# Kernel optimization log

Measured on AMD Instinct MI355X. Metric: run time of the kernel, lower is better.

## Reference

```python
import jax, jax.numpy as jnp
import numpy as np

ENT_SIZE = 1_000_000
REL_SIZE = 1_000
ENT_DIM = 128
REL_DIM = 128  # == ENT_DIM, so eye(rel_dim, ent_dim) is the identity
BATCH = 262_144
MARGIN = 1.0
EPS = 1e-6  # nn.PairwiseDistance default eps, added to the difference


def setup_inputs() -> dict:
    key = jax.random.key(0)
    k1, k2, k3, k4, k5, k6, k7, k8 = jax.random.split(key, 8)
    scale = 0.05
    ent_emb = jax.random.normal(k1, (ENT_SIZE, ENT_DIM), jnp.float32) * scale
    ent_map_emb = jax.random.normal(k2, (ENT_SIZE, ENT_DIM), jnp.float32) * scale
    rel_emb = jax.random.normal(k3, (REL_SIZE, REL_DIM), jnp.float32) * scale
    rel_map_emb = jax.random.normal(k4, (REL_SIZE, REL_DIM), jnp.float32) * scale

    def make_triples(ke, kr):
        ents = jax.random.randint(ke, (BATCH, 2), 0, ENT_SIZE, jnp.int32)
        rels = jax.random.randint(kr, (BATCH, 1), 0, REL_SIZE, jnp.int32)
        # columns: head, relation, tail
        return jnp.concatenate([ents[:, :1], rels, ents[:, 1:]], axis=1)

    pos_x = make_triples(k5, k6)
    neg_x = make_triples(k7, k8)
    return {
        "ent_emb": ent_emb,
        "ent_map_emb": ent_map_emb,
        "rel_emb": rel_emb,
        "rel_map_emb": rel_map_emb,
        "pos_x": pos_x,
        "neg_x": neg_x,
    }


def _score(ent_emb, ent_map_emb, rel_emb, rel_map_emb, triple):
    h, r, t = triple[:, 0], triple[:, 1], triple[:, 2]
    head = ent_emb[h]          # [B, D]
    headp = ent_map_emb[h]     # [B, D]
    tail = ent_emb[t]
    tailp = ent_map_emb[t]
    rel = rel_emb[r]           # [B, D]
    relp = rel_map_emb[r]      # [B, D]
    # Mrh = relp[:, :, None] @ headp[:, None, :] + I ; Mrh @ head
    # == relp * <headp, head> + head   (since REL_DIM == ENT_DIM => I@head = head)
    head_proj = relp * jnp.sum(headp * head, axis=-1, keepdims=True) + head
    tail_proj = relp * jnp.sum(tailp * tail, axis=-1, keepdims=True) + tail
    d = head_proj + rel - tail_proj + EPS  # PairwiseDistance adds eps to diff
    return jnp.sqrt(jnp.sum(d * d, axis=-1))  # L2 norm (l_regular=2), [B]


def reference(ent_emb, ent_map_emb, rel_emb, rel_map_emb, pos_x, neg_x):
    pos_score = _score(ent_emb, ent_map_emb, rel_emb, rel_map_emb, pos_x)
    neg_score = _score(ent_emb, ent_map_emb, rel_emb, rel_map_emb, neg_x)
    size = pos_x.shape[0]
    return jnp.sum(jax.nn.relu(pos_score - neg_score + MARGIN)) / size
```

## Files before the change

kernel.cpp:

```cpp
#include <hip/hip_runtime.h>

#define ENT_DIM 128
#define BATCH 262144
#define MARGIN 1.0f
#define EPS 1e-6f

__global__ void zero_out_kernel(float* out) {
    out[0] = 0.0f;
}

__global__ __launch_bounds__(256) void transd_kernel(
    const float* __restrict__ ent_emb,
    const float* __restrict__ ent_map,
    const float* __restrict__ rel_emb,
    const float* __restrict__ rel_map,
    const int* __restrict__ pos_x,
    const int* __restrict__ neg_x,
    float* __restrict__ out)
{
    const int lane = threadIdx.x & 63;
    const int wid  = threadIdx.x >> 6;
    const int gwave  = blockIdx.x * 4 + wid;
    const int nwaves = gridDim.x * 4;

    float acc = 0.0f;

    for (int i = gwave; i < BATCH; i += nwaves) {
        const int ib = __builtin_amdgcn_readfirstlane(i);

        const int ph = pos_x[3 * ib + 0];
        const int pr = pos_x[3 * ib + 1];
        const int pt = pos_x[3 * ib + 2];
        const int nh = neg_x[3 * ib + 0];
        const int nr = neg_x[3 * ib + 1];
        const int nt = neg_x[3 * ib + 2];

        const float2 phe = ((const float2*)(ent_emb + (size_t)ph * ENT_DIM))[lane];
        const float2 phm = ((const float2*)(ent_map + (size_t)ph * ENT_DIM))[lane];
        const float2 pte = ((const float2*)(ent_emb + (size_t)pt * ENT_DIM))[lane];
        const float2 ptm = ((const float2*)(ent_map + (size_t)pt * ENT_DIM))[lane];
        const float2 pre = ((const float2*)(rel_emb + (size_t)pr * ENT_DIM))[lane];
        const float2 prm = ((const float2*)(rel_map + (size_t)pr * ENT_DIM))[lane];

        const float2 nhe = ((const float2*)(ent_emb + (size_t)nh * ENT_DIM))[lane];
        const float2 nhm = ((const float2*)(ent_map + (size_t)nh * ENT_DIM))[lane];
        const float2 nte = ((const float2*)(ent_emb + (size_t)nt * ENT_DIM))[lane];
        const float2 ntm = ((const float2*)(ent_map + (size_t)nt * ENT_DIM))[lane];
        const float2 nre = ((const float2*)(rel_emb + (size_t)nr * ENT_DIM))[lane];
        const float2 nrm = ((const float2*)(rel_map + (size_t)nr * ENT_DIM))[lane];

        float dph = phm.x * phe.x + phm.y * phe.y;
        float dpt = ptm.x * pte.x + ptm.y * pte.y;
        float dnh = nhm.x * nhe.x + nhm.y * nhe.y;
        float dnt = ntm.x * nte.x + ntm.y * nte.y;

        #pragma unroll
        for (int off = 32; off >= 1; off >>= 1) {
            dph += __shfl_xor(dph, off);
            dpt += __shfl_xor(dpt, off);
            dnh += __shfl_xor(dnh, off);
            dnt += __shfl_xor(dnt, off);
        }

        float dpx = prm.x * dph + phe.x + pre.x - (prm.x * dpt + pte.x) + EPS;
        float dpy = prm.y * dph + phe.y + pre.y - (prm.y * dpt + pte.y) + EPS;
        float dnx = nrm.x * dnh + nhe.x + nre.x - (nrm.x * dnt + nte.x) + EPS;
        float dny = nrm.y * dnh + nhe.y + nre.y - (nrm.y * dnt + nte.y) + EPS;

        float sp = dpx * dpx + dpy * dpy;
        float sn = dnx * dnx + dny * dny;

        #pragma unroll
        for (int off = 32; off >= 1; off >>= 1) {
            sp += __shfl_xor(sp, off);
            sn += __shfl_xor(sn, off);
        }

        float v = sqrtf(sp) - sqrtf(sn) + MARGIN;
        acc += fmaxf(v, 0.0f);
    }

    __shared__ float wsum[4];
    if (lane == 0) wsum[wid] = acc;
    __syncthreads();
    if (threadIdx.x == 0) {
        float s = wsum[0] + wsum[1] + wsum[2] + wsum[3];
        atomicAdd(out, s * (1.0f / (float)BATCH));
    }
}

extern "C" void kernel_launch(void* const* d_in, const int* in_sizes, int n_in,
                              void* d_out, int out_size, void* d_ws, size_t ws_size,
                              hipStream_t stream) {
    const float* ent_emb     = (const float*)d_in[0];
    const float* ent_map_emb = (const float*)d_in[1];
    const float* rel_emb     = (const float*)d_in[2];
    const float* rel_map_emb = (const float*)d_in[3];
    const int*   pos_x       = (const int*)d_in[4];
    const int*   neg_x       = (const int*)d_in[5];
    float* out = (float*)d_out;

    hipLaunchKernelGGL(zero_out_kernel, dim3(1), dim3(1), 0, stream, out);

    hipLaunchKernelGGL(transd_kernel, dim3(4096), dim3(256), 0, stream,
                       ent_emb, ent_map_emb, rel_emb, rel_map_emb,
                       pos_x, neg_x, out);
}
```

Baseline: 936.2 us.

## Split wave into pos/neg halves with float4 loads and double-buffered prefetch

Each wave now handles one triple per half-wave: lanes 0-31 take the positive triple and lanes 32-63 the negative one, and each lane loads float4 slices. The wave loads all 16 triples' indices for its contiguous chunk in one vector load and hands them out by shuffle. Embedding loads for the next iteration are issued before the current pair is computed, which keeps more gathers in flight to hide latency. In exchange register pressure rises from the doubled buffers, and the grid is now fixed by batch size instead of a grid-stride loop.

```diff
diff --git a/kernel.cpp b/kernel.cpp
--- a/kernel.cpp
+++ b/kernel.cpp
@@ -4,12 +4,58 @@
 #define BATCH 262144
 #define MARGIN 1.0f
 #define EPS 1e-6f
+#define NITER 16
+#define WAVES_PER_BLOCK 4
+#define NWAVES (BATCH / NITER)
+#define NBLOCKS (NWAVES / WAVES_PER_BLOCK)
 
 __global__ void zero_out_kernel(float* out) {
     out[0] = 0.0f;
 }
 
-__global__ __launch_bounds__(256) void transd_kernel(
+__device__ __forceinline__ float pair_term(
+    float4 H, float4 Hp, float4 T, float4 Tp, float4 R, float4 Rp, int lane)
+{
+    float dh = H.x*Hp.x + H.y*Hp.y + H.z*Hp.z + H.w*Hp.w;
+    float dt = T.x*Tp.x + T.y*Tp.y + T.z*Tp.z + T.w*Tp.w;
+#pragma unroll
+    for (int off = 16; off >= 1; off >>= 1) {
+        dh += __shfl_xor(dh, off);
+        dt += __shfl_xor(dt, off);
+    }
+
+    float dx = Rp.x * dh + H.x + R.x - (Rp.x * dt + T.x) + EPS;
+    float dy = Rp.y * dh + H.y + R.y - (Rp.y * dt + T.y) + EPS;
+    float dz = Rp.z * dh + H.z + R.z - (Rp.z * dt + T.z) + EPS;
+    float dw = Rp.w * dh + H.w + R.w - (Rp.w * dt + T.w) + EPS;
+
+    float s = dx*dx + dy*dy + dz*dz + dw*dw;
+#pragma unroll
+    for (int off = 16; off >= 1; off >>= 1) s += __shfl_xor(s, off);
+
+    float so = __shfl_xor(s, 32);
+    float a = sqrtf(s), b = sqrtf(so);
+    float v = (lane < 32) ? (a - b) : (b - a);
+    return fmaxf(v + MARGIN, 0.0f);
+}
+
+#define LOADP(kk, p) do {                                                   \
+    const int e0 = 3*(kk), e1 = 3*(kk) + 1, e2 = 3*(kk) + 2;                \
+    int ih = __shfl((e0 & 1) ? ivy : ivx, (e0 >> 1) + hi32);                \
+    int ir = __shfl((e1 & 1) ? ivy : ivx, (e1 >> 1) + hi32);                \
+    int it = __shfl((e2 & 1) ? ivy : ivx, (e2 >> 1) + hi32);                \
+    uint ho = ((uint)ih << 9) | lofs;                                       \
+    uint ro = ((uint)ir << 9) | lofs;                                       \
+    uint to = ((uint)it << 9) | lofs;                                       \
+    H##p  = *(const float4*)(eb + ho);                                      \
+    Hp##p = *(const float4*)(em + ho);                                      \
+    T##p  = *(const float4*)(eb + to);                                      \
+    Tp##p = *(const float4*)(em + to);                                      \
+    R##p  = *(const float4*)(rb + ro);                                      \
+    Rp##p = *(const float4*)(rm + ro);                                      \
+} while (0)
+
+__global__ __launch_bounds__(256, 4) void transd_kernel(
     const float* __restrict__ ent_emb,
     const float* __restrict__ ent_map,
     const float* __restrict__ rel_emb,
@@ -20,67 +66,39 @@
 {
     const int lane = threadIdx.x & 63;
     const int wid  = threadIdx.x >> 6;
-    const int gwave  = blockIdx.x * 4 + wid;
-    const int nwaves = gridDim.x * 4;
+    const int gw   = blockIdx.x * WAVES_PER_BLOCK + wid;
 
+    const int  hi32 = lane & 32;
+    const uint lofs = (uint)(lane & 31) << 4;
+
+    const char* __restrict__ eb = (const char*)ent_emb;
+    const char* __restrict__ em = (const char*)ent_map;
+    const char* __restrict__ rb = (const char*)rel_emb;
+    const char* __restrict__ rm = (const char*)rel_map;
+
+    int ivx = 0, ivy = 0;
+    if (lane < 24) {
+        int2 t = ((const int2*)(pos_x + 3 * NITER * gw))[lane];
+        ivx = t.x; ivy = t.y;
+    } else if (hi32 && lane < 56) {
+        int2 t = ((const int2*)(neg_x + 3 * NITER * gw))[lane - 32];
+        ivx = t.x; ivy = t.y;
+    }
+
+    float4 H0, Hp0, T0, Tp0, R0, Rp0;
+    float4 H1, Hp1, T1, Tp1, R1, Rp1;
     float acc = 0.0f;
 
-    for (int i = gwave; i < BATCH; i += nwaves) {
-        const int ib = __builtin_amdgcn_readfirstlane(i);
-
-        const int ph = pos_x[3 * ib + 0];
-        const int pr = pos_x[3 * ib + 1];
-        const int pt = pos_x[3 * ib + 2];
-        const int nh = neg_x[3 * ib + 0];
-        const int nr = neg_x[3 * ib + 1];
-        const int nt = neg_x[3 * ib + 2];
-
-        const float2 phe = ((const float2*)(ent_emb + (size_t)ph * ENT_DIM))[lane];
-        const float2 phm = ((const float2*)(ent_map + (size_t)ph * ENT_DIM))[lane];
-        const float2 pte = ((const float2*)(ent_emb + (size_t)pt * ENT_DIM))[lane];
-        const float2 ptm = ((const float2*)(ent_map + (size_t)pt * ENT_DIM))[lane];
-        const float2 pre = ((const float2*)(rel_emb + (size_t)pr * ENT_DIM))[lane];
-        const float2 prm = ((const float2*)(rel_map + (size_t)pr * ENT_DIM))[lane];
-
-        const float2 nhe = ((const float2*)(ent_emb + (size_t)nh * ENT_DIM))[lane];
-        const float2 nhm = ((const float2*)(ent_map + (size_t)nh * ENT_DIM))[lane];
-        const float2 nte = ((const float2*)(ent_emb + (size_t)nt * ENT_DIM))[lane];
-        const float2 ntm = ((const float2*)(ent_map + (size_t)nt * ENT_DIM))[lane];
-        const float2 nre = ((const float2*)(rel_emb + (size_t)nr * ENT_DIM))[lane];
-        const float2 nrm = ((const float2*)(rel_map + (size_t)nr * ENT_DIM))[lane];
-
-        float dph = phm.x * phe.x + phm.y * phe.y;
-        float dpt = ptm.x * pte.x + ptm.y * pte.y;
-        float dnh = nhm.x * nhe.x + nhm.y * nhe.y;
-        float dnt = ntm.x * nte.x + ntm.y * nte.y;
-
-        #pragma unroll
-        for (int off = 32; off >= 1; off >>= 1) {
-            dph += __shfl_xor(dph, off);
-            dpt += __shfl_xor(dpt, off);
-            dnh += __shfl_xor(dnh, off);
-            dnt += __shfl_xor(dnt, off);
-        }
-
-        float dpx = prm.x * dph + phe.x + pre.x - (prm.x * dpt + pte.x) + EPS;
-        float dpy = prm.y * dph + phe.y + pre.y - (prm.y * dpt + pte.y) + EPS;
-        float dnx = nrm.x * dnh + nhe.x + nre.x - (nrm.x * dnt + nte.x) + EPS;
-        float dny = nrm.y * dnh + nhe.y + nre.y - (nrm.y * dnt + nte.y) + EPS;
-
-        float sp = dpx * dpx + dpy * dpy;
-        float sn = dnx * dnx + dny * dny;
-
-        #pragma unroll
-        for (int off = 32; off >= 1; off >>= 1) {
-            sp += __shfl_xor(sp, off);
-            sn += __shfl_xor(sn, off);
-        }
-
-        float v = sqrtf(sp) - sqrtf(sn) + MARGIN;
-        acc += fmaxf(v, 0.0f);
+    LOADP(0, 0);
+#pragma unroll
+    for (int k = 0; k < NITER; k += 2) {
+        LOADP(k + 1, 1);
+        acc += pair_term(H0, Hp0, T0, Tp0, R0, Rp0, lane);
+        if (k + 2 < NITER) LOADP(k + 2, 0);
+        acc += pair_term(H1, Hp1, T1, Tp1, R1, Rp1, lane);
     }
 
-    __shared__ float wsum[4];
+    __shared__ float wsum[WAVES_PER_BLOCK];
     if (lane == 0) wsum[wid] = acc;
     __syncthreads();
     if (threadIdx.x == 0) {
@@ -102,7 +120,7 @@
 
     hipLaunchKernelGGL(zero_out_kernel, dim3(1), dim3(1), 0, stream, out);
 
-    hipLaunchKernelGGL(transd_kernel, dim3(4096), dim3(256), 0, stream,
+    hipLaunchKernelGGL(transd_kernel, dim3(NBLOCKS), dim3(256), 0, stream,
                        ent_emb, ent_map_emb, rel_emb, rel_map_emb,
                        pos_x, neg_x, out);
 }
```

Result: no change. 928.4 us (-0.8%).
